# Performance work log

Measured on AMD Instinct MI355X. Metric: run time of the kernel, lower is better.

Reference implementation:

```python
import jax, jax.numpy as jnp
import numpy as np

N_NODES = 100000


def gcn_conv(x, src, dst, ew, W, b):
    """PyG GCNConv: linear transform, add self-loops, symmetric degree
    normalization with edge weights, scatter-add aggregation, then bias."""
    n = x.shape[0]
    h = x @ W  # [N, out] transform BEFORE propagation (PyG order)
    # add self-loops with weight 1
    loop = jnp.arange(n, dtype=src.dtype)
    s = jnp.concatenate([src, loop])
    d = jnp.concatenate([dst, loop])
    w = jnp.concatenate([ew, jnp.ones((n,), dtype=ew.dtype)])
    # symmetric normalization: deg computed over incoming edge weights
    deg = jax.ops.segment_sum(w, d, num_segments=n)
    dinv = jnp.where(deg > 0, jax.lax.rsqrt(deg), 0.0)
    norm = dinv[s] * w * dinv[d]  # [E+N]
    msg = h[s] * norm[:, None]  # gather + scale
    out = jax.ops.segment_sum(msg, d, num_segments=n)  # scatter-add
    return out + b


def setup_inputs() -> dict:
    key = jax.random.key(0)
    k = jax.random.split(key, 6)
    N, E, F, H, C = N_NODES, 3200000, 512, 16, 40
    x = jax.random.normal(k[0], (N, F), dtype=jnp.float32)
    edge_index = jax.random.randint(k[1], (2, E), 0, N, dtype=jnp.int64)
    edge_weight = jax.random.uniform(k[2], (E,), dtype=jnp.float32)
    W1 = jax.random.normal(k[3], (F, H), dtype=jnp.float32) * (1.0 / np.sqrt(F))
    b1 = jnp.zeros((H,), dtype=jnp.float32)
    W2 = jax.random.normal(k[4], (H, C), dtype=jnp.float32) * (1.0 / np.sqrt(H))
    b2 = jnp.zeros((C,), dtype=jnp.float32)
    return {"x": x, "edge_index": edge_index, "edge_weight": edge_weight,
            "W1": W1, "b1": b1, "W2": W2, "b2": b2}


def reference(x, edge_index, edge_weight, W1, b1, W2, b2):
    src, dst = edge_index[0], edge_index[1]
    h = jax.nn.relu(gcn_conv(x, src, dst, edge_weight, W1, b1))
    # F.dropout with training=False (eval) is identity -> omitted
    h = gcn_conv(h, src, dst, edge_weight, W2, b2)
    return jax.nn.log_softmax(h, axis=1)
```

## Files before the change

### kernel.cpp

```cpp
#include <hip/hip_runtime.h>


#define NF 512
#define NH 16
#define NRANGE 32
#define NS2 32
#define RS 3125
#define EB 1024
#define GROWS 256
#define GK 16

__device__ __forceinline__ unsigned short f2bf(float f) {
    unsigned u = __float_as_uint(f);
    return (unsigned short)((u + 0x7fff + ((u >> 16) & 1)) >> 16);
}
__device__ __forceinline__ float bf2f(unsigned b) {
    return __uint_as_float(b << 16);
}


__global__ __launch_bounds__(256) void k_bincount(const int* __restrict__ dst,
                                                  int* __restrict__ bktcnt,
                                                  int E, int nblk) {
    __shared__ int cnt[NRANGE];
    if (threadIdx.x < NRANGE) cnt[threadIdx.x] = 0;
    __syncthreads();
    int b0 = blockIdx.x * EB;
#pragma unroll
    for (int j = 0; j < 4; ++j) {
        int e = b0 + j * 256 + threadIdx.x;
        if (e < E) atomicAdd(&cnt[dst[e] / RS], 1);
    }
    __syncthreads();
    if (threadIdx.x < NRANGE)
        bktcnt[threadIdx.x * nblk + blockIdx.x] = cnt[threadIdx.x];
}

__global__ __launch_bounds__(256) void k_scan_block(const int* __restrict__ in,
                                                    int* __restrict__ outp,
                                                    int* __restrict__ bsum, int n) {
    __shared__ int sh[256];
    int t = threadIdx.x, g = blockIdx.x * 256 + t;
    int v = (g < n) ? in[g] : 0;
    sh[t] = v; __syncthreads();
    for (int off = 1; off < 256; off <<= 1) {
        int a = (t >= off) ? sh[t - off] : 0;
        __syncthreads();
        sh[t] += a;
        __syncthreads();
    }
    if (g < n) outp[g] = sh[t] - v;
    if (t == 255) bsum[blockIdx.x] = sh[255];
}

__global__ __launch_bounds__(256) void k_sumscan(const unsigned* __restrict__ partials,
                                                 int* __restrict__ rowptr,
                                                 int* __restrict__ bsum,
                                                 float* __restrict__ dinv, int n) {
    __shared__ int sh[256];
    int t = threadIdx.x, g = blockIdx.x * 256 + t;
    int v = 0;
    if (g < n) {
        int r = g / RS, b = g - r * RS;
        const unsigned* p = partials + (size_t)(r * NS2) * RS + b;
        unsigned wq = 0;
#pragma unroll
        for (int s = 0; s < NS2; ++s) {
            unsigned pk = p[s * RS];
            v += (int)(pk >> 25);
            wq += pk & 0x1ffffffu;
        }
        dinv[g] = rsqrtf(1.0f + (float)wq * (1.0f / 1024.0f));
    }
    sh[t] = v; __syncthreads();
    for (int off = 1; off < 256; off <<= 1) {
        int a = (t >= off) ? sh[t - off] : 0;
        __syncthreads();
        sh[t] += a;
        __syncthreads();
    }
    if (g < n) rowptr[g] = sh[t] - v;
    if (t == 255) bsum[blockIdx.x] = sh[255];
}

__global__ __launch_bounds__(512) void k_scan_tops(int* __restrict__ bsum,
                                                   int* __restrict__ outp,
                                                   int nb, int n) {
    __shared__ int sh[512];
    int t = threadIdx.x;
    int v = (t < nb) ? bsum[t] : 0;
    sh[t] = v; __syncthreads();
    for (int off = 1; off < 512; off <<= 1) {
        int a = (t >= off) ? sh[t - off] : 0;
        __syncthreads();
        sh[t] += a;
        __syncthreads();
    }
    if (t < nb) bsum[t] = sh[t] - v;
    if (t == 511) outp[n] = sh[511];
}

__global__ __launch_bounds__(256) void k_scan_add(int* __restrict__ outp,
                                                  const int* __restrict__ bsum, int n) {
    int i = blockIdx.x * 256 + threadIdx.x;
    if (i < n) outp[i] += bsum[i >> 8];
}

__global__ __launch_bounds__(256) void k_binfill(const int* __restrict__ src,
                                                 const int* __restrict__ dst,
                                                 const float* __restrict__ ew,
                                                 const int* __restrict__ bktcnt,
                                                 const int* __restrict__ bsum2,
                                                 int2* __restrict__ bin,
                                                 int E, int nblk) {
    __shared__ int base[NRANGE];
    if (threadIdx.x < NRANGE) {
        int idx = threadIdx.x * nblk + blockIdx.x;
        base[threadIdx.x] = bktcnt[idx] + bsum2[idx >> 8];
    }
    __syncthreads();
    int b0 = blockIdx.x * EB;
#pragma unroll
    for (int j = 0; j < 4; ++j) {
        int e = b0 + j * 256 + threadIdx.x;
        if (e < E) {
            int d = dst[e];
            int r = d / RS;
            int pos = atomicAdd(&base[r], 1);
            bin[pos] = make_int2((src[e] << 12) | (d - r * RS),
                                 __float_as_int(ew[e]));
        }
    }
}

__device__ __forceinline__ int bkt_start(const int* bktcnt, const int* bsum2,
                                         int r, int nblk, int E) {
    if (r >= NRANGE) return E;
    int idx = r * nblk;
    return bktcnt[idx] + bsum2[idx >> 8];
}

__global__ __launch_bounds__(256) void k_hist2(const int2* __restrict__ bin,
                                               const int* __restrict__ bktcnt,
                                               const int* __restrict__ bsum2,
                                               unsigned* __restrict__ partials,
                                               int E, int nblk) {
    __shared__ unsigned hist[RS];
    int r = blockIdx.x >> 5, s = blockIdx.x & (NS2 - 1);
    for (int t = threadIdx.x; t < RS; t += 256) hist[t] = 0;
    __syncthreads();
    int b0 = bkt_start(bktcnt, bsum2, r, nblk, E);
    int b1 = bkt_start(bktcnt, bsum2, r + 1, nblk, E);
    int len = b1 - b0, ss = (len + NS2 - 1) / NS2;
    int cs = b0 + s * ss, ce = min(cs + ss, b1);
    for (int j = cs + threadIdx.x; j < ce; j += 256) {
        int2 p2 = bin[j];
        unsigned wq = (unsigned)(__int_as_float(p2.y) * 1024.0f + 0.5f);
        atomicAdd(&hist[p2.x & 4095], (1u << 25) | wq);
    }
    __syncthreads();
    unsigned* pp = partials + (size_t)(r * NS2 + s) * RS;
    for (int t = threadIdx.x; t < RS; t += 256) pp[t] = hist[t];
}

__global__ __launch_bounds__(256) void k_slicecur(unsigned* __restrict__ partials,
                                                  const int* __restrict__ rowptr, int n) {
    int d = blockIdx.x * 256 + threadIdx.x;
    if (d >= n) return;
    int r = d / RS, b = d - r * RS;
    unsigned* p = partials + (size_t)(r * NS2) * RS + b;
    int run = rowptr[d];
#pragma unroll
    for (int s = 0; s < NS2; ++s) {
        int c = (int)(p[s * RS] >> 25);
        p[s * RS] = (unsigned)run;
        run += c;
    }
}

__global__ __launch_bounds__(256) void k_fill3(const int2* __restrict__ bin,
                                               const int* __restrict__ bktcnt,
                                               const int* __restrict__ bsum2,
                                               const unsigned* __restrict__ partials,
                                               const float* __restrict__ dinv,
                                               unsigned* __restrict__ csr,
                                               int E, int nblk) {
    __shared__ int cur[RS];
    __shared__ float dv[RS];
    int r = blockIdx.x >> 5, s = blockIdx.x & (NS2 - 1);
    const unsigned* cp = partials + (size_t)(r * NS2 + s) * RS;
    for (int t = threadIdx.x; t < RS; t += 256) {
        cur[t] = (int)cp[t];
        dv[t] = dinv[r * RS + t];
    }
    __syncthreads();
    int b0 = bkt_start(bktcnt, bsum2, r, nblk, E);
    int b1 = bkt_start(bktcnt, bsum2, r + 1, nblk, E);
    int len = b1 - b0, ss = (len + NS2 - 1) / NS2;
    int cs = b0 + s * ss, ce = min(cs + ss, b1);
    for (int j = cs + threadIdx.x; j < ce; j += 256) {
        int2 p2 = bin[j];
        int dl = p2.x & 4095;
        int sn = p2.x >> 12;
        float nrm = dinv[sn] * __int_as_float(p2.y) * dv[dl];
        unsigned w15 = (unsigned)(nrm * 32767.0f + 0.5f);
        int pos = atomicAdd(&cur[dl], 1);
        csr[pos] = ((unsigned)sn << 15) | w15;
    }
}

__global__ __launch_bounds__(256) void k_gemm1(const float* __restrict__ x,
                                               const float* __restrict__ w1,
                                               unsigned short* __restrict__ h, int n) {
    __shared__ unsigned wtb[NF * NH / 2];
    __shared__ float xs[2][GROWS * GK];
    for (int idx = threadIdx.x; idx < NF * NH / 2; idx += 256) {
        int k4 = idx >> 5, rem = idx & 31;
        int f = rem >> 1, kk = (rem & 1) * 2;
        float v0 = w1[(k4 * 4 + kk) * NH + f];
        float v1 = w1[(k4 * 4 + kk + 1) * NH + f];
        wtb[idx] = (unsigned)f2bf(v0) | ((unsigned)f2bf(v1) << 16);
    }
    int rq = threadIdx.x >> 2;
    int fq = threadIdx.x & 3;
    int base = blockIdx.x * GROWS;
    float4 stage[4];
#define LOAD_CHUNK(kc)                                                        \
    _Pragma("unroll")                                                         \
    for (int li = 0; li < 4; ++li) {                                          \
        int idx = li * 256 + threadIdx.x;                                     \
        int row = idx >> 2, c4 = idx & 3;                                     \
        int rg = base + row; if (rg > n - 1) rg = n - 1;                      \
        stage[li] = *(const float4*)(x + (size_t)rg * NF + (kc) * GK + c4 * 4);\
    }
#define WRITE_CHUNK(b)                                                        \
    _Pragma("unroll")                                                         \
    for (int li = 0; li < 4; ++li) {                                          \
        int idx = li * 256 + threadIdx.x;                                     \
        int row = idx >> 2, c4 = idx & 3;                                     \
        int slot = (c4 + (row >> 2)) & 3;                                     \
        float* p = &xs[b][row * GK + slot * 4];                               \
        p[0] = stage[li].x; p[1] = stage[li].y;                               \
        p[2] = stage[li].z; p[3] = stage[li].w;                               \
    }
    float acc[4][4] = {{0.f}};
    LOAD_CHUNK(0)
    WRITE_CHUNK(0)
    __syncthreads();
    for (int kc = 0; kc < NF / GK; ++kc) {
        if (kc + 1 < NF / GK) { LOAD_CHUNK(kc + 1) }
        int b = kc & 1;
#pragma unroll
        for (int k4c = 0; k4c < GK / 4; ++k4c) {
            int k4 = kc * (GK / 4) + k4c;
            float4 wf[4];
#pragma unroll
            for (int c = 0; c < 4; ++c) {
                uint2 u = *(const uint2*)&wtb[k4 * 32 + (fq * 4 + c) * 2];
                wf[c].x = __uint_as_float(u.x << 16);
                wf[c].y = __uint_as_float(u.x & 0xffff0000u);
                wf[c].z = __uint_as_float(u.y << 16);
                wf[c].w = __uint_as_float(u.y & 0xffff0000u);
            }
#pragma unroll
            for (int i = 0; i < 4; ++i) {
                int row = rq * 4 + i;
                int slot = (k4c + rq) & 3;
                float4 xv = *(const float4*)&xs[b][row * GK + slot * 4];
#pragma unroll
                for (int c = 0; c < 4; ++c) {
                    acc[i][c] = fmaf(xv.x, wf[c].x, acc[i][c]);
                    acc[i][c] = fmaf(xv.y, wf[c].y, acc[i][c]);
                    acc[i][c] = fmaf(xv.z, wf[c].z, acc[i][c]);
                    acc[i][c] = fmaf(xv.w, wf[c].w, acc[i][c]);
                }
            }
        }
        if (kc + 1 < NF / GK) {
            __syncthreads();
            WRITE_CHUNK((kc + 1) & 1)
            __syncthreads();
        }
    }
#pragma unroll
    for (int i = 0; i < 4; ++i) {
        int r = base + rq * 4 + i;
        if (r < n) {
            ushort4 o;
            o.x = f2bf(acc[i][0]); o.y = f2bf(acc[i][1]);
            o.z = f2bf(acc[i][2]); o.w = f2bf(acc[i][3]);
            *(ushort4*)(h + (size_t)r * NH + fq * 4) = o;
        }
    }
#undef LOAD_CHUNK
#undef WRITE_CHUNK
}

template <bool RELU>
__global__ __launch_bounds__(256) void k_gatherT(const unsigned short* __restrict__ in,
                                                 const float* __restrict__ dinv,
                                                 const int* __restrict__ rowptr,
                                                 const unsigned* __restrict__ csr,
                                                 const float* __restrict__ b1,
                                                 unsigned short* __restrict__ out, int n) {
    int tid = blockIdx.x * 256 + threadIdx.x;
    int d = tid >> 3, l = tid & 7;
    if (d >= n) return;
    float di = dinv[d];
    unsigned self = *(const unsigned*)(in + (size_t)d * NH + 2 * l);
    float a0 = bf2f(self & 0xffffu) * di * di;
    float a1 = bf2f(self >> 16) * di * di;
    int e0 = rowptr[d], e1 = rowptr[d + 1];
    for (int j = e0; j < e1; ++j) {
        unsigned e = csr[j];
        float nrm = (float)(e & 32767u) * (1.0f / 32767.0f);
        unsigned pr = *(const unsigned*)(in + (size_t)(e >> 15) * NH + 2 * l);
        a0 = fmaf(bf2f(pr & 0xffffu), nrm, a0);
        a1 = fmaf(bf2f(pr >> 16), nrm, a1);
    }
    if (RELU) {
        a0 = fmaxf(a0 + b1[2 * l], 0.0f);
        a1 = fmaxf(a1 + b1[2 * l + 1], 0.0f);
    }
    unsigned pk = (unsigned)f2bf(a0) | ((unsigned)f2bf(a1) << 16);
    *(unsigned*)(out + (size_t)d * NH + 2 * l) = pk;
}

__global__ __launch_bounds__(256) void k_out(const unsigned short* __restrict__ agg,
                                             const float* __restrict__ w2,
                                             const float* __restrict__ b2,
                                             float* __restrict__ out, int n) {
    __shared__ float w2s[NH * 40];
    __shared__ float b2s[40];
    for (int t = threadIdx.x; t < NH * 40; t += 256) w2s[t] = w2[t];
    if (threadIdx.x < 40) b2s[threadIdx.x] = b2[threadIdx.x];
    __syncthreads();
    int i = blockIdx.x * 256 + threadIdx.x;
    if (i >= n) return;
    float v[NH];
    const uint4* ap = (const uint4*)(agg + (size_t)i * NH);
#pragma unroll
    for (int m = 0; m < 2; ++m) {
        uint4 q = ap[m];
        v[8 * m + 0] = bf2f(q.x & 0xffffu); v[8 * m + 1] = bf2f(q.x >> 16);
        v[8 * m + 2] = bf2f(q.y & 0xffffu); v[8 * m + 3] = bf2f(q.y >> 16);
        v[8 * m + 4] = bf2f(q.z & 0xffffu); v[8 * m + 5] = bf2f(q.z >> 16);
        v[8 * m + 6] = bf2f(q.w & 0xffffu); v[8 * m + 7] = bf2f(q.w >> 16);
    }
    float z[40];
#pragma unroll
    for (int c = 0; c < 40; ++c) {
        float a = b2s[c];
#pragma unroll
        for (int ff = 0; ff < NH; ++ff) a = fmaf(v[ff], w2s[ff * 40 + c], a);
        z[c] = a;
    }
    float mx = z[0];
#pragma unroll
    for (int c = 1; c < 40; ++c) mx = fmaxf(mx, z[c]);
    float sum = 0.0f;
#pragma unroll
    for (int c = 0; c < 40; ++c) sum += expf(z[c] - mx);
    float ls = mx + logf(sum);
    float4* op = (float4*)(out + (size_t)i * 40);
#pragma unroll
    for (int m = 0; m < 10; ++m) {
        float4 o;
        o.x = z[4 * m] - ls; o.y = z[4 * m + 1] - ls;
        o.z = z[4 * m + 2] - ls; o.w = z[4 * m + 3] - ls;
        op[m] = o;
    }
}

extern "C" void kernel_launch(void* const* d_in, const int* in_sizes, int n_in,
                              void* d_out, int out_size, void* d_ws, size_t ws_size,
                              hipStream_t stream) {
    const float* x  = (const float*)d_in[0];
    const int*   ei = (const int*)d_in[1];
    const float* ew = (const float*)d_in[2];
    const float* w1 = (const float*)d_in[3];
    const float* b1 = (const float*)d_in[4];
    const float* w2 = (const float*)d_in[5];
    const float* b2 = (const float*)d_in[6];
    float* out = (float*)d_out;

    int n = in_sizes[0] / NF;
    int E = in_sizes[2];
    const int* src = ei;
    const int* dst = ei + E;

    float*          ws       = (float*)d_ws;
    float*          dinv     = ws;
    int*            bsum     = (int*)(ws + 200000);
    int*            rowptr   = (int*)(ws + 201024);
    int*            bsum2    = (int*)(ws + 301056);
    int*            bktcnt   = (int*)(ws + 302080);
    unsigned*       partials = (unsigned*)(ws + 402112);
    unsigned*       csr      = (unsigned*)(ws + 6802112);
    int2*           bin      = (int2*)(ws + 10002112);
    unsigned short* h        = (unsigned short*)(ws + 10002112);
    unsigned short* o1       = (unsigned short*)(ws + 10802112);

    int nblk  = (E + EB - 1) / EB;
    int ncnt  = NRANGE * nblk;
    int nb_c  = (ncnt + 255) / 256;
    int nb_n  = (n + 255) / 256;
    int nb_g8 = (n * 8 + 255) / 256;
    int nb_g  = (n + GROWS - 1) / GROWS;

    k_bincount<<<nblk, 256, 0, stream>>>(dst, bktcnt, E, nblk);
    k_scan_block<<<nb_c, 256, 0, stream>>>(bktcnt, bktcnt, bsum2, ncnt);
    k_scan_tops<<<1, 512, 0, stream>>>(bsum2, bktcnt, nb_c, ncnt);
    k_binfill<<<nblk, 256, 0, stream>>>(src, dst, ew, bktcnt, bsum2, bin, E, nblk);
    k_hist2<<<NRANGE * NS2, 256, 0, stream>>>(bin, bktcnt, bsum2, partials, E, nblk);
    k_sumscan<<<nb_n, 256, 0, stream>>>(partials, rowptr, bsum, dinv, n);
    k_scan_tops<<<1, 512, 0, stream>>>(bsum, rowptr, nb_n, n);
    k_scan_add<<<nb_n, 256, 0, stream>>>(rowptr, bsum, n);
    k_slicecur<<<nb_n, 256, 0, stream>>>(partials, rowptr, n);
    k_fill3<<<NRANGE * NS2, 256, 0, stream>>>(bin, bktcnt, bsum2, partials,
                                              dinv, csr, E, nblk);
    k_gemm1<<<nb_g, 256, 0, stream>>>(x, w1, h, n);
    k_gatherT<true><<<nb_g8, 256, 0, stream>>>(h, dinv, rowptr, csr, b1, o1, n);
    k_gatherT<false><<<nb_g8, 256, 0, stream>>>(o1, dinv, rowptr, csr, b1, h, n);
    k_out<<<nb_n, 256, 0, stream>>>(h, w2, b2, out, n);
}
```

Baseline: 279.2 us.

## Fuse second gather with output projection and fold scan-add into consumers

Removes the separate scan-add pass by adding block offsets on the fly wherever rowptr is read. Fuses the second aggregation with the W2 projection and log-softmax, spreading the 40 classes across 8 lanes with shuffles, which removes one kernel launch and the intermediate bf16 round trip. It also halves the GEMM1 rows per block and replaces the swizzled shared-memory layout with a padded stride, which gives more blocks. The costs are extra index arithmetic in the gather loops and scalar rather than vectorized output stores.

```diff
diff --git a/kernel.cpp b/kernel.cpp
--- a/kernel.cpp
+++ b/kernel.cpp
@@ -7,8 +7,9 @@
 #define NS2 32
 #define RS 3125
 #define EB 1024
-#define GROWS 256
+#define GROWS 128
 #define GK 16
+#define XST 20
 
 __device__ __forceinline__ unsigned short f2bf(float f) {
     unsigned u = __float_as_uint(f);
@@ -17,7 +18,6 @@
 __device__ __forceinline__ float bf2f(unsigned b) {
     return __uint_as_float(b << 16);
 }
-
 
 __global__ __launch_bounds__(256) void k_bincount(const int* __restrict__ dst,
                                                   int* __restrict__ bktcnt,
@@ -100,12 +100,6 @@
     if (t == 511) outp[n] = sh[511];
 }
 
-__global__ __launch_bounds__(256) void k_scan_add(int* __restrict__ outp,
-                                                  const int* __restrict__ bsum, int n) {
-    int i = blockIdx.x * 256 + threadIdx.x;
-    if (i < n) outp[i] += bsum[i >> 8];
-}
-
 __global__ __launch_bounds__(256) void k_binfill(const int* __restrict__ src,
                                                  const int* __restrict__ dst,
                                                  const float* __restrict__ ew,
@@ -164,12 +158,13 @@
 }
 
 __global__ __launch_bounds__(256) void k_slicecur(unsigned* __restrict__ partials,
-                                                  const int* __restrict__ rowptr, int n) {
+                                                  const int* __restrict__ rowptr,
+                                                  const int* __restrict__ bsum, int n) {
     int d = blockIdx.x * 256 + threadIdx.x;
     if (d >= n) return;
     int r = d / RS, b = d - r * RS;
     unsigned* p = partials + (size_t)(r * NS2) * RS + b;
-    int run = rowptr[d];
+    int run = rowptr[d] + bsum[d >> 8];
 #pragma unroll
     for (int s = 0; s < NS2; ++s) {
         int c = (int)(p[s * RS] >> 25);
@@ -213,7 +208,7 @@
                                                const float* __restrict__ w1,
                                                unsigned short* __restrict__ h, int n) {
     __shared__ unsigned wtb[NF * NH / 2];
-    __shared__ float xs[2][GROWS * GK];
+    __shared__ float xs[2][GROWS * XST];
     for (int idx = threadIdx.x; idx < NF * NH / 2; idx += 256) {
         int k4 = idx >> 5, rem = idx & 31;
         int f = rem >> 1, kk = (rem & 1) * 2;
@@ -224,10 +219,10 @@
     int rq = threadIdx.x >> 2;
     int fq = threadIdx.x & 3;
     int base = blockIdx.x * GROWS;
-    float4 stage[4];
+    float4 stage[2];
 #define LOAD_CHUNK(kc)                                                        \
     _Pragma("unroll")                                                         \
-    for (int li = 0; li < 4; ++li) {                                          \
+    for (int li = 0; li < 2; ++li) {                                          \
         int idx = li * 256 + threadIdx.x;                                     \
         int row = idx >> 2, c4 = idx & 3;                                     \
         int rg = base + row; if (rg > n - 1) rg = n - 1;                      \
@@ -235,15 +230,14 @@
     }
 #define WRITE_CHUNK(b)                                                        \
     _Pragma("unroll")                                                         \
-    for (int li = 0; li < 4; ++li) {                                          \
+    for (int li = 0; li < 2; ++li) {                                          \
         int idx = li * 256 + threadIdx.x;                                     \
         int row = idx >> 2, c4 = idx & 3;                                     \
-        int slot = (c4 + (row >> 2)) & 3;                                     \
-        float* p = &xs[b][row * GK + slot * 4];                               \
+        float* p = &xs[b][row * XST + c4 * 4];                                \
         p[0] = stage[li].x; p[1] = stage[li].y;                               \
         p[2] = stage[li].z; p[3] = stage[li].w;                               \
     }
-    float acc[4][4] = {{0.f}};
+    float acc[2][4] = {{0.f}};
     LOAD_CHUNK(0)
     WRITE_CHUNK(0)
     __syncthreads();
@@ -263,10 +257,9 @@
                 wf[c].w = __uint_as_float(u.y & 0xffff0000u);
             }
 #pragma unroll
-            for (int i = 0; i < 4; ++i) {
-                int row = rq * 4 + i;
-                int slot = (k4c + rq) & 3;
-                float4 xv = *(const float4*)&xs[b][row * GK + slot * 4];
+            for (int i = 0; i < 2; ++i) {
+                int row = rq * 2 + i;
+                float4 xv = *(const float4*)&xs[b][row * XST + k4c * 4];
 #pragma unroll
                 for (int c = 0; c < 4; ++c) {
                     acc[i][c] = fmaf(xv.x, wf[c].x, acc[i][c]);
@@ -283,8 +276,8 @@
         }
     }
 #pragma unroll
-    for (int i = 0; i < 4; ++i) {
-        int r = base + rq * 4 + i;
+    for (int i = 0; i < 2; ++i) {
+        int r = base + rq * 2 + i;
         if (r < n) {
             ushort4 o;
             o.x = f2bf(acc[i][0]); o.y = f2bf(acc[i][1]);
@@ -296,13 +289,13 @@
 #undef WRITE_CHUNK
 }
 
-template <bool RELU>
-__global__ __launch_bounds__(256) void k_gatherT(const unsigned short* __restrict__ in,
-                                                 const float* __restrict__ dinv,
-                                                 const int* __restrict__ rowptr,
-                                                 const unsigned* __restrict__ csr,
-                                                 const float* __restrict__ b1,
-                                                 unsigned short* __restrict__ out, int n) {
+__global__ __launch_bounds__(256) void k_gather_relu(const unsigned short* __restrict__ in,
+                                                     const float* __restrict__ dinv,
+                                                     const int* __restrict__ rowptr,
+                                                     const int* __restrict__ bsum,
+                                                     const unsigned* __restrict__ csr,
+                                                     const float* __restrict__ b1,
+                                                     unsigned short* __restrict__ out, int n) {
     int tid = blockIdx.x * 256 + threadIdx.x;
     int d = tid >> 3, l = tid & 7;
     if (d >= n) return;
@@ -310,7 +303,8 @@
     unsigned self = *(const unsigned*)(in + (size_t)d * NH + 2 * l);
     float a0 = bf2f(self & 0xffffu) * di * di;
     float a1 = bf2f(self >> 16) * di * di;
-    int e0 = rowptr[d], e1 = rowptr[d + 1];
+    int e0 = rowptr[d] + bsum[d >> 8];
+    int e1 = (d + 1 < n) ? rowptr[d + 1] + bsum[(d + 1) >> 8] : rowptr[n];
     for (int j = e0; j < e1; ++j) {
         unsigned e = csr[j];
         float nrm = (float)(e & 32767u) * (1.0f / 32767.0f);
@@ -318,58 +312,70 @@
         a0 = fmaf(bf2f(pr & 0xffffu), nrm, a0);
         a1 = fmaf(bf2f(pr >> 16), nrm, a1);
     }
-    if (RELU) {
-        a0 = fmaxf(a0 + b1[2 * l], 0.0f);
-        a1 = fmaxf(a1 + b1[2 * l + 1], 0.0f);
-    }
+    a0 = fmaxf(a0 + b1[2 * l], 0.0f);
+    a1 = fmaxf(a1 + b1[2 * l + 1], 0.0f);
     unsigned pk = (unsigned)f2bf(a0) | ((unsigned)f2bf(a1) << 16);
     *(unsigned*)(out + (size_t)d * NH + 2 * l) = pk;
 }
 
-__global__ __launch_bounds__(256) void k_out(const unsigned short* __restrict__ agg,
-                                             const float* __restrict__ w2,
-                                             const float* __restrict__ b2,
-                                             float* __restrict__ out, int n) {
+__global__ __launch_bounds__(256) void k_gather_out(const unsigned short* __restrict__ in,
+                                                    const float* __restrict__ dinv,
+                                                    const int* __restrict__ rowptr,
+                                                    const int* __restrict__ bsum,
+                                                    const unsigned* __restrict__ csr,
+                                                    const float* __restrict__ w2,
+                                                    const float* __restrict__ b2,
+                                                    float* __restrict__ out, int n) {
     __shared__ float w2s[NH * 40];
     __shared__ float b2s[40];
     for (int t = threadIdx.x; t < NH * 40; t += 256) w2s[t] = w2[t];
     if (threadIdx.x < 40) b2s[threadIdx.x] = b2[threadIdx.x];
     __syncthreads();
-    int i = blockIdx.x * 256 + threadIdx.x;
-    if (i >= n) return;
+    int tid = blockIdx.x * 256 + threadIdx.x;
+    int d = tid >> 3, l = tid & 7;
+    if (d >= n) return;
+    float di = dinv[d];
+    unsigned self = *(const unsigned*)(in + (size_t)d * NH + 2 * l);
+    float a0 = bf2f(self & 0xffffu) * di * di;
+    float a1 = bf2f(self >> 16) * di * di;
+    int e0 = rowptr[d] + bsum[d >> 8];
+    int e1 = (d + 1 < n) ? rowptr[d + 1] + bsum[(d + 1) >> 8] : rowptr[n];
+    for (int j = e0; j < e1; ++j) {
+        unsigned e = csr[j];
+        float nrm = (float)(e & 32767u) * (1.0f / 32767.0f);
+        unsigned pr = *(const unsigned*)(in + (size_t)(e >> 15) * NH + 2 * l);
+        a0 = fmaf(bf2f(pr & 0xffffu), nrm, a0);
+        a1 = fmaf(bf2f(pr >> 16), nrm, a1);
+    }
     float v[NH];
-    const uint4* ap = (const uint4*)(agg + (size_t)i * NH);
-#pragma unroll
-    for (int m = 0; m < 2; ++m) {
-        uint4 q = ap[m];
-        v[8 * m + 0] = bf2f(q.x & 0xffffu); v[8 * m + 1] = bf2f(q.x >> 16);
-        v[8 * m + 2] = bf2f(q.y & 0xffffu); v[8 * m + 3] = bf2f(q.y >> 16);
-        v[8 * m + 4] = bf2f(q.z & 0xffffu); v[8 * m + 5] = bf2f(q.z >> 16);
-        v[8 * m + 6] = bf2f(q.w & 0xffffu); v[8 * m + 7] = bf2f(q.w >> 16);
-    }
-    float z[40];
-#pragma unroll
-    for (int c = 0; c < 40; ++c) {
+#pragma unroll
+    for (int m = 0; m < 8; ++m) {
+        v[2 * m] = __shfl(a0, m, 8);
+        v[2 * m + 1] = __shfl(a1, m, 8);
+    }
+    float z[5];
+#pragma unroll
+    for (int j5 = 0; j5 < 5; ++j5) {
+        int c = l * 5 + j5;
         float a = b2s[c];
 #pragma unroll
         for (int ff = 0; ff < NH; ++ff) a = fmaf(v[ff], w2s[ff * 40 + c], a);
-        z[c] = a;
+        z[j5] = a;
     }
     float mx = z[0];
 #pragma unroll
-    for (int c = 1; c < 40; ++c) mx = fmaxf(mx, z[c]);
+    for (int j5 = 1; j5 < 5; ++j5) mx = fmaxf(mx, z[j5]);
+#pragma unroll
+    for (int off = 4; off; off >>= 1) mx = fmaxf(mx, __shfl_xor(mx, off, 8));
     float sum = 0.0f;
 #pragma unroll
-    for (int c = 0; c < 40; ++c) sum += expf(z[c] - mx);
+    for (int j5 = 0; j5 < 5; ++j5) sum += expf(z[j5] - mx);
+#pragma unroll
+    for (int off = 4; off; off >>= 1) sum += __shfl_xor(sum, off, 8);
     float ls = mx + logf(sum);
-    float4* op = (float4*)(out + (size_t)i * 40);
-#pragma unroll
-    for (int m = 0; m < 10; ++m) {
-        float4 o;
-        o.x = z[4 * m] - ls; o.y = z[4 * m + 1] - ls;
-        o.z = z[4 * m + 2] - ls; o.w = z[4 * m + 3] - ls;
-        op[m] = o;
-    }
+    float* op = out + (size_t)d * 40 + l * 5;
+#pragma unroll
+    for (int j5 = 0; j5 < 5; ++j5) op[j5] = z[j5] - ls;
 }
 
 extern "C" void kernel_launch(void* const* d_in, const int* in_sizes, int n_in,
@@ -415,12 +421,10 @@
     k_hist2<<<NRANGE * NS2, 256, 0, stream>>>(bin, bktcnt, bsum2, partials, E, nblk);
     k_sumscan<<<nb_n, 256, 0, stream>>>(partials, rowptr, bsum, dinv, n);
     k_scan_tops<<<1, 512, 0, stream>>>(bsum, rowptr, nb_n, n);
-    k_scan_add<<<nb_n, 256, 0, stream>>>(rowptr, bsum, n);
-    k_slicecur<<<nb_n, 256, 0, stream>>>(partials, rowptr, n);
+    k_slicecur<<<nb_n, 256, 0, stream>>>(partials, rowptr, bsum, n);
     k_fill3<<<NRANGE * NS2, 256, 0, stream>>>(bin, bktcnt, bsum2, partials,
                                               dinv, csr, E, nblk);
     k_gemm1<<<nb_g, 256, 0, stream>>>(x, w1, h, n);
-    k_gatherT<true><<<nb_g8, 256, 0, stream>>>(h, dinv, rowptr, csr, b1, o1, n);
-    k_gatherT<false><<<nb_g8, 256, 0, stream>>>(o1, dinv, rowptr, csr, b1, h, n);
-    k_out<<<nb_n, 256, 0, stream>>>(h, w2, b2, out, n);
-}
+    k_gather_relu<<<nb_g8, 256, 0, stream>>>(h, dinv, rowptr, bsum, csr, b1, o1, n);
+    k_gather_out<<<nb_g8, 256, 0, stream>>>(o1, dinv, rowptr, bsum, csr, w2, b2, out, n);
+}
```

Measured after the change: 269.4 us. 1.04x faster.
